# Kernel optimization log

Measured on AMD Instinct MI355X. Metric: run time of the kernel, lower is better.

## Reference

```python
import jax, jax.numpy as jnp
import numpy as np

B, T, E, H, V, A = 128, 31, 512, 512, 10000, 2048


def _lstm_step(h, c, x, W_ih, W_hh, b_ih, b_hh):
    # PyTorch LSTM gate order: i, f, g, o
    gates = x @ W_ih.T + h @ W_hh.T + b_ih + b_hh  # [B, 4H]
    i, f, g, o = jnp.split(gates, 4, axis=-1)
    i = jax.nn.sigmoid(i)
    f = jax.nn.sigmoid(f)
    g = jnp.tanh(g)
    o = jax.nn.sigmoid(o)
    c2 = f * c + i * g
    h2 = o * jnp.tanh(c2)
    return h2, c2


def setup_inputs() -> dict:
    key = jax.random.key(0)
    ks = jax.random.split(key, 16)
    s = 0.1                      # uniform_(-0.1, 0.1) init in the module
    k = 1.0 / np.sqrt(H)         # PyTorch LSTM default init
    u = lambda kk, shape, a: jax.random.uniform(kk, shape, jnp.float32, -a, a)
    return {
        "features": jax.random.normal(ks[0], (B, E), jnp.float32),
        "cnn_features": jax.random.uniform(ks[1], (B, A), jnp.float32),
        "captions": jax.random.randint(ks[2], (B, T), 0, V),
        "lengths": jnp.full((B,), T + 1, dtype=jnp.int32),
        "embed_table": u(ks[3], (V, E), s),
        "W_ih": u(ks[4], (4 * H, E), k),
        "W_hh": u(ks[5], (4 * H, H), k),
        "b_ih": u(ks[6], (4 * H,), k),
        "b_hh": u(ks[7], (4 * H,), k),
        "W_attn": u(ks[8], (A, H + E), s),
        "b_attn": jnp.zeros((A,), jnp.float32),
        "W_attd": u(ks[9], (E, A + E), s),
        "b_attd": jnp.zeros((E,), jnp.float32),
        "W_out": u(ks[10], (V, H), s),
        "b_out": jnp.zeros((V,), jnp.float32),
    }


def reference(features, cnn_features, captions, lengths, embed_table,
              W_ih, W_hh, b_ih, b_hh, W_attn, b_attn, W_attd, b_attd,
              W_out, b_out):
    # embeddings with image feature prepended: [B, T+1, E]
    emb = embed_table[captions]
    xs = jnp.concatenate([features[:, None, :], emb], axis=1)

    # timestep 0: plain LSTM step from zero state (no attention)
    h0 = jnp.zeros((B, H), xs.dtype)
    c0 = jnp.zeros((B, H), xs.dtype)
    h1, c1 = _lstm_step(h0, c0, xs[:, 0], W_ih, W_hh, b_ih, b_hh)

    def step(carry, x_t):
        h, c = carry
        info = jnp.concatenate([x_t, h], axis=-1)                    # [B, E+H]
        aw = jax.nn.softmax(info @ W_attn.T + b_attn, axis=-1)       # [B, 2048]
        attended = cnn_features * aw                                  # [B, 2048]
        x2 = jnp.concatenate([x_t, attended], axis=-1) @ W_attd.T + b_attd  # [B, E]
        h2, c2 = _lstm_step(h, c, x2, W_ih, W_hh, b_ih, b_hh)
        return (h2, c2), h2

    xs_rest = jnp.swapaxes(xs[:, 1:], 0, 1)          # [T, B, E]
    _, hs = jax.lax.scan(step, (h1, c1), xs_rest)    # [T, B, H]

    hidden = jnp.concatenate([h1[None], hs], axis=0)  # [T+1, B, H] packed order
    hidden = hidden.reshape(-1, H)                    # [(T+1)*B, H]
    logits = hidden @ W_out.T + b_out                 # [(T+1)*B, V]
    return logits
```

## Files before the change

### kernel.cpp

```cpp
#include <hip/hip_runtime.h>

#define B_ 128
#define T_ 31
#define E_ 512
#define H_ 512
#define V_ 10000
#define A_ 2048
#define TP1 32
#define G4 2048
#define NHC 4096
#define MPRE 3968

typedef unsigned short u16;
typedef __attribute__((ext_vector_type(8))) short bf16x8;
typedef __attribute__((ext_vector_type(4))) float f32x4;

__device__ __forceinline__ u16 f2b(float f) {
  union { float f; unsigned u; } x; x.f = f;
  unsigned r = x.u + 0x7fffu + ((x.u >> 16) & 1u);
  return (u16)(r >> 16);
}
__device__ __forceinline__ float sigmoidf_(float x) { return 1.f / (1.f + __expf(-x)); }


__global__ __launch_bounds__(256) void prep_xs(
    u16* __restrict__ xs, const float* __restrict__ features,
    const int* __restrict__ captions, const float* __restrict__ embed) {
  int idx = blockIdx.x * 256 + threadIdx.x;
  int e = idx & 511;
  int b = (idx >> 9) & 127;
  int t = idx >> 16;
  float v;
  if (t == 0) v = features[b * 512 + e];
  else        v = embed[(size_t)captions[b * 31 + (t - 1)] * 512 + e];
  xs[idx] = f2b(v);
}

__global__ __launch_bounds__(256) void cast_k(
    u16* __restrict__ dst, const float* __restrict__ src, int n) {
  int i = blockIdx.x * 256 + threadIdx.x;
  if (i < n) dst[i] = f2b(src[i]);
}

__global__ __launch_bounds__(256) void prep_attn_w(
    u16* __restrict__ WattnE, u16* __restrict__ WhComb, const float* __restrict__ W_attn) {
  int i = blockIdx.x * 256 + threadIdx.x;
  int r = i >> 9, k = i & 511;
  WattnE[i] = f2b(W_attn[r * 1024 + k]);
  WhComb[i] = f2b(W_attn[r * 1024 + 512 + k]);
}

__global__ __launch_bounds__(256) void prep_attdE(
    u16* __restrict__ dst, const float* __restrict__ W_attd) {
  int i = blockIdx.x * 256 + threadIdx.x;
  int r = i >> 9, k = i & 511;
  dst[i] = f2b(W_attd[r * 2560 + k]);
}

__global__ __launch_bounds__(256) void prep_attdAT(
    u16* __restrict__ dst, const float* __restrict__ W_attd) {
  int i = blockIdx.x * 256 + threadIdx.x;
  int a = i >> 9, e = i & 511;
  dst[i] = f2b(W_attd[(size_t)e * 2560 + 512 + a]);
}

__global__ __launch_bounds__(256) void add_bias2(
    float* __restrict__ dst, const float* __restrict__ a, const float* __restrict__ b) {
  int i = blockIdx.x * 256 + threadIdx.x;
  if (i < G4) dst[i] = a[i] + b[i];
}

template<bool OUT_BF16, bool ATOMIC, bool NGUARD>
__global__ __launch_bounds__(256) void gemm_nt(
    const u16* __restrict__ Ag, const u16* __restrict__ Bg,
    void* __restrict__ Cout, const float* __restrict__ bias,
    int N, int lda, int ldb, int ldc, int kChunk) {
  __shared__ __align__(16) u16 As[64 * 40];
  __shared__ __align__(16) u16 Bs[64 * 40];
  const int n0 = blockIdx.x * 64;
  const int m0 = blockIdx.y * 64;
  const int k0 = blockIdx.z * kChunk;
  const int tid  = threadIdx.x;
  const int wave = tid >> 6, lane = tid & 63;
  const int quad = lane >> 4, lq = lane & 15;
  const int srow = tid >> 2, sgrp = tid & 3;

  f32x4 acc[4] = {{0,0,0,0},{0,0,0,0},{0,0,0,0},{0,0,0,0}};
  const u16* aptr = Ag + (size_t)(m0 + srow) * lda + k0 + sgrp * 8;
  const u16* bptr = Bg + (size_t)(n0 + srow) * ldb + k0 + sgrp * 8;
  const bool bvalid = !NGUARD || (n0 + srow) < N;

  for (int kk = 0; kk < kChunk; kk += 32) {
    uint4 av = *(const uint4*)(aptr + kk);
    uint4 bv = make_uint4(0u, 0u, 0u, 0u);
    if (bvalid) bv = *(const uint4*)(bptr + kk);
    __syncthreads();
    *(uint4*)&As[srow * 40 + sgrp * 8] = av;
    *(uint4*)&Bs[srow * 40 + sgrp * 8] = bv;
    __syncthreads();
    bf16x8 af = *(const bf16x8*)&As[(wave * 16 + lq) * 40 + quad * 8];
#pragma unroll
    for (int j = 0; j < 4; ++j) {
      bf16x8 bfr = *(const bf16x8*)&Bs[(j * 16 + lq) * 40 + quad * 8];
      acc[j] = __builtin_amdgcn_mfma_f32_16x16x32_bf16(af, bfr, acc[j], 0, 0, 0);
    }
  }
  const int row = m0 + wave * 16 + quad * 4;
#pragma unroll
  for (int j = 0; j < 4; ++j) {
    int col = n0 + j * 16 + lq;
    if (NGUARD && col >= N) continue;
    float bval = bias ? bias[col] : 0.f;
#pragma unroll
    for (int r = 0; r < 4; ++r) {
      float v = acc[j][r] + bval;
      size_t ci = (size_t)(row + r) * ldc + col;
      if (OUT_BF16)      ((u16*)Cout)[ci] = f2b(v);
      else if (ATOMIC)   atomicAdd((float*)Cout + ci, v);
      else               ((float*)Cout)[ci] = v;
    }
  }
}


__global__ __launch_bounds__(256) void attn_softmax(
    const float* __restrict__ preA_t, const float* __restrict__ hW,
    const float* __restrict__ cnn, u16* __restrict__ att, float* __restrict__ g2) {
  int b = blockIdx.x, tid = threadIdx.x;
  float e[8]; float sum = 0.f;
#pragma unroll
  for (int i = 0; i < 8; ++i) {
    int n = tid + i * 256;
    float s = preA_t[b * 2048 + n] + hW[b * 4096 + n];
    e[i] = __expf(s);
    sum += e[i];
  }
#pragma unroll
  for (int o = 32; o > 0; o >>= 1) sum += __shfl_down(sum, o);
  __shared__ float wsum[4];
  if ((tid & 63) == 0) wsum[tid >> 6] = sum;
  __syncthreads();
  float inv = 1.f / (wsum[0] + wsum[1] + wsum[2] + wsum[3]);
#pragma unroll
  for (int i = 0; i < 8; ++i) {
    int n = tid + i * 256;
    att[b * 2048 + n] = f2b(cnn[b * 2048 + n] * e[i] * inv);
    g2[b * 2048 + n] = 0.f;
  }
}

__global__ __launch_bounds__(256) void lstm_pw(
    const float* __restrict__ gA, int ldA,
    const float* __restrict__ gB, const float* __restrict__ gC,
    float* __restrict__ c_st, u16* __restrict__ h_out, int first) {
  int idx = blockIdx.x * 256 + threadIdx.x;
  int b = idx >> 9, j = idx & 511;
  size_t ra = (size_t)b * ldA;
  float gi = gA[ra + j], gf = gA[ra + 512 + j], gg = gA[ra + 1024 + j], go = gA[ra + 1536 + j];
  if (gB) {
    size_t rb = (size_t)b * 4096 + 2048;
    gi += gB[rb + j]; gf += gB[rb + 512 + j]; gg += gB[rb + 1024 + j]; go += gB[rb + 1536 + j];
  }
  if (gC) {
    size_t rc = (size_t)b * 2048;
    gi += gC[rc + j]; gf += gC[rc + 512 + j]; gg += gC[rc + 1024 + j]; go += gC[rc + 1536 + j];
  }
  float iv = sigmoidf_(gi), fv = sigmoidf_(gf), gv = tanhf(gg), ov = sigmoidf_(go);
  float cp = first ? 0.f : c_st[idx];
  float cn = fv * cp + iv * gv;
  c_st[idx] = cn;
  h_out[idx] = f2b(ov * tanhf(cn));
}


extern "C" void kernel_launch(void* const* d_in, const int* in_sizes, int n_in,
                              void* d_out, int out_size, void* d_ws, size_t ws_size,
                              hipStream_t stream) {
  (void)in_sizes; (void)n_in; (void)out_size; (void)ws_size;
  const float* features = (const float*)d_in[0];
  const float* cnn      = (const float*)d_in[1];
  const int*   captions = (const int*)d_in[2];
  const float* embed    = (const float*)d_in[4];
  const float* W_ih     = (const float*)d_in[5];
  const float* W_hh     = (const float*)d_in[6];
  const float* b_ih     = (const float*)d_in[7];
  const float* b_hh     = (const float*)d_in[8];
  const float* W_attn   = (const float*)d_in[9];
  const float* b_attn   = (const float*)d_in[10];
  const float* W_attd   = (const float*)d_in[11];
  const float* b_attd   = (const float*)d_in[12];
  const float* W_out    = (const float*)d_in[13];
  const float* b_out    = (const float*)d_in[14];

  char* ws = (char*)d_ws;
  size_t off = 0;
  auto alloc = [&](size_t bytes) { void* p = ws + off; off += (bytes + 255) & ~255UL; return p; };
  u16*   xs_tb   = (u16*)  alloc((size_t)TP1 * B_ * E_ * 2);
  u16*   h_all   = (u16*)  alloc((size_t)TP1 * B_ * H_ * 2);
  u16*   Wh_comb = (u16*)  alloc((size_t)NHC * H_ * 2);
  u16*   W_ih_b  = (u16*)  alloc((size_t)G4 * E_ * 2);
  u16*   W_attnE = (u16*)  alloc((size_t)A_ * E_ * 2);
  u16*   W_attdE = (u16*)  alloc((size_t)E_ * E_ * 2);
  u16*   W_attdAT= (u16*)  alloc((size_t)A_ * E_ * 2);
  u16*   W_out_b = (u16*)  alloc((size_t)V_ * H_ * 2);
  u16*   Wc      = (u16*)  alloc((size_t)G4 * A_ * 2);
  u16*   pre_x2  = (u16*)  alloc((size_t)MPRE * E_ * 2);
  float* c_st    = (float*)alloc((size_t)B_ * H_ * 4);
  float* hW      = (float*)alloc((size_t)B_ * NHC * 4);
  float* g2      = (float*)alloc((size_t)B_ * G4 * 4);
  u16*   att     = (u16*)  alloc((size_t)B_ * A_ * 2);
  float* bias_c  = (float*)alloc((size_t)G4 * 4);

  float* preA = (float*)d_out;
  float* preG = preA + (size_t)MPRE * A_;
  float* logits = (float*)d_out;

  prep_xs<<<(TP1 * B_ * E_) / 256, 256, 0, stream>>>(xs_tb, features, captions, embed);
  cast_k<<<(G4 * E_) / 256, 256, 0, stream>>>(W_ih_b, W_ih, G4 * E_);
  cast_k<<<(V_ * H_) / 256, 256, 0, stream>>>(W_out_b, W_out, V_ * H_);
  cast_k<<<(G4 * H_) / 256, 256, 0, stream>>>(Wh_comb + (size_t)A_ * H_, W_hh, G4 * H_);
  prep_attn_w<<<(A_ * E_) / 256, 256, 0, stream>>>(W_attnE, Wh_comb, W_attn);
  prep_attdE<<<(E_ * E_) / 256, 256, 0, stream>>>(W_attdE, W_attd);
  prep_attdAT<<<(A_ * E_) / 256, 256, 0, stream>>>(W_attdAT, W_attd);
  add_bias2<<<G4 / 256, 256, 0, stream>>>(bias_c, b_ih, b_hh);

  gemm_nt<true, false, false><<<dim3(A_ / 64, G4 / 64, 1), 256, 0, stream>>>(
      W_ih_b, W_attdAT, Wc, nullptr, A_, 512, 512, A_, 512);
  gemm_nt<false, false, false><<<dim3(A_ / 64, MPRE / 64, 1), 256, 0, stream>>>(
      xs_tb + (size_t)B_ * E_, W_attnE, preA, b_attn, A_, 512, 512, A_, 512);
  gemm_nt<true, false, false><<<dim3(E_ / 64, MPRE / 64, 1), 256, 0, stream>>>(
      xs_tb + (size_t)B_ * E_, W_attdE, pre_x2, b_attd, E_, 512, 512, E_, 512);
  gemm_nt<false, false, false><<<dim3(G4 / 64, MPRE / 64, 1), 256, 0, stream>>>(
      pre_x2, W_ih_b, preG, bias_c, G4, 512, 512, G4, 512);
  gemm_nt<false, false, false><<<dim3(G4 / 64, B_ / 64, 1), 256, 0, stream>>>(
      xs_tb, W_ih_b, g2, bias_c, G4, 512, 512, G4, 512);
  lstm_pw<<<(B_ * H_) / 256, 256, 0, stream>>>(g2, G4, nullptr, nullptr, c_st, h_all, 1);

  for (int t = 1; t <= T_; ++t) {
    gemm_nt<false, false, false><<<dim3(NHC / 64, B_ / 64, 1), 256, 0, stream>>>(
        h_all + (size_t)(t - 1) * B_ * H_, Wh_comb, hW, nullptr, NHC, 512, 512, NHC, 512);
    attn_softmax<<<B_, 256, 0, stream>>>(
        preA + (size_t)(t - 1) * B_ * A_, hW, cnn, att, g2);
    gemm_nt<false, true, false><<<dim3(G4 / 64, B_ / 64, 4), 256, 0, stream>>>(
        att, Wc, g2, nullptr, G4, A_, A_, G4, 512);
    lstm_pw<<<(B_ * H_) / 256, 256, 0, stream>>>(
        preG + (size_t)(t - 1) * B_ * G4, G4, hW, g2, c_st,
        h_all + (size_t)t * B_ * H_, 0);
  }

  gemm_nt<false, false, true><<<dim3((V_ + 63) / 64, (TP1 * B_) / 64, 1), 256, 0, stream>>>(
      h_all, W_out_b, logits, b_out, V_, 512, 512, V_, 512);
}
```

Measured before the change: 1.247 ms.

## Fuse recurrent timestep loop into one persistent kernel with grid barriers

Replaces the 31-step host loop of four launches per step (h GEMM, softmax, attention GEMM with atomics, pointwise LSTM) with a single persistent 256-block kernel. Inside it the steps are separated by software grid barriers on an atomic counter. Gate weights and biases are permuted so each block owns 4 gates of a hidden unit, which lets the attention GEMM reduce through LDS and keep the cell state in registers. This removes about 124 launches and the atomics. The cost is spin-wait barriers, which rely on all 256 blocks being co-resident; this is not guaranteed.

Result: slower. 3.937 ms (+215.7%).

```diff
diff --git a/kernel.cpp b/kernel.cpp
--- a/kernel.cpp
+++ b/kernel.cpp
@@ -42,6 +42,14 @@
   if (i < n) dst[i] = f2b(src[i]);
 }
 
+__global__ __launch_bounds__(256) void prep_w_perm(
+    u16* __restrict__ dst, const float* __restrict__ W) {
+  int i = blockIdx.x * 256 + threadIdx.x;
+  int gp = i >> 9, k = i & 511;
+  int j = gp >> 2, gate = gp & 3;
+  dst[i] = f2b(W[((size_t)gate * 512 + j) * 512 + k]);
+}
+
 __global__ __launch_bounds__(256) void prep_attn_w(
     u16* __restrict__ WattnE, u16* __restrict__ WhComb, const float* __restrict__ W_attn) {
   int i = blockIdx.x * 256 + threadIdx.x;
@@ -64,10 +72,14 @@
   dst[i] = f2b(W_attd[(size_t)e * 2560 + 512 + a]);
 }
 
-__global__ __launch_bounds__(256) void add_bias2(
+__global__ __launch_bounds__(256) void prep_bias_p(
     float* __restrict__ dst, const float* __restrict__ a, const float* __restrict__ b) {
   int i = blockIdx.x * 256 + threadIdx.x;
-  if (i < G4) dst[i] = a[i] + b[i];
+  if (i < G4) {
+    int j = i >> 2, gate = i & 3;
+    int g = gate * 512 + j;
+    dst[i] = a[g] + b[g];
+  }
 }
 
 template<bool OUT_BF16, bool ATOMIC, bool NGUARD>
@@ -122,54 +134,130 @@
   }
 }
 
-
-__global__ __launch_bounds__(256) void attn_softmax(
-    const float* __restrict__ preA_t, const float* __restrict__ hW,
-    const float* __restrict__ cnn, u16* __restrict__ att, float* __restrict__ g2) {
-  int b = blockIdx.x, tid = threadIdx.x;
-  float e[8]; float sum = 0.f;
-#pragma unroll
-  for (int i = 0; i < 8; ++i) {
-    int n = tid + i * 256;
-    float s = preA_t[b * 2048 + n] + hW[b * 4096 + n];
-    e[i] = __expf(s);
-    sum += e[i];
-  }
-#pragma unroll
-  for (int o = 32; o > 0; o >>= 1) sum += __shfl_down(sum, o);
-  __shared__ float wsum[4];
-  if ((tid & 63) == 0) wsum[tid >> 6] = sum;
-  __syncthreads();
-  float inv = 1.f / (wsum[0] + wsum[1] + wsum[2] + wsum[3]);
-#pragma unroll
-  for (int i = 0; i < 8; ++i) {
-    int n = tid + i * 256;
-    att[b * 2048 + n] = f2b(cnn[b * 2048 + n] * e[i] * inv);
-    g2[b * 2048 + n] = 0.f;
-  }
-}
-
-__global__ __launch_bounds__(256) void lstm_pw(
-    const float* __restrict__ gA, int ldA,
-    const float* __restrict__ gB, const float* __restrict__ gC,
-    float* __restrict__ c_st, u16* __restrict__ h_out, int first) {
+__global__ __launch_bounds__(256) void lstm0_pw(
+    const float* __restrict__ g0, float* __restrict__ c_st, u16* __restrict__ h0) {
   int idx = blockIdx.x * 256 + threadIdx.x;
   int b = idx >> 9, j = idx & 511;
-  size_t ra = (size_t)b * ldA;
-  float gi = gA[ra + j], gf = gA[ra + 512 + j], gg = gA[ra + 1024 + j], go = gA[ra + 1536 + j];
-  if (gB) {
-    size_t rb = (size_t)b * 4096 + 2048;
-    gi += gB[rb + j]; gf += gB[rb + 512 + j]; gg += gB[rb + 1024 + j]; go += gB[rb + 1536 + j];
-  }
-  if (gC) {
-    size_t rc = (size_t)b * 2048;
-    gi += gC[rc + j]; gf += gC[rc + 512 + j]; gg += gC[rc + 1024 + j]; go += gC[rc + 1536 + j];
-  }
-  float iv = sigmoidf_(gi), fv = sigmoidf_(gf), gv = tanhf(gg), ov = sigmoidf_(go);
-  float cp = first ? 0.f : c_st[idx];
-  float cn = fv * cp + iv * gv;
-  c_st[idx] = cn;
-  h_out[idx] = f2b(ov * tanhf(cn));
+  float4 g = *(const float4*)&g0[(size_t)b * 2048 + j * 4];
+  float iv = sigmoidf_(g.x), gv = tanhf(g.z), ov = sigmoidf_(g.w);
+  float c = iv * gv;
+  c_st[idx] = c;
+  h0[idx] = f2b(ov * tanhf(c));
+}
+
+
+__device__ __forceinline__ void grid_barrier(unsigned* ctr, unsigned target) {
+  __syncthreads();
+  if (threadIdx.x == 0) {
+    __threadfence();
+    __hip_atomic_fetch_add(ctr, 1u, __ATOMIC_RELAXED, __HIP_MEMORY_SCOPE_AGENT);
+    while (__hip_atomic_load(ctr, __ATOMIC_RELAXED, __HIP_MEMORY_SCOPE_AGENT) < target)
+      __builtin_amdgcn_s_sleep(1);
+  }
+  __syncthreads();
+  __threadfence();
+}
+
+__global__ __launch_bounds__(256) void recurrence(
+    const u16* __restrict__ Whc, const u16* __restrict__ Wc,
+    const float* __restrict__ preA, const float* __restrict__ preG,
+    const float* __restrict__ cnn, const float* __restrict__ c_init,
+    u16* __restrict__ h_all, float* __restrict__ hW, u16* __restrict__ att,
+    unsigned* __restrict__ ctr) {
+  __shared__ float red[4 * 64 * 17];
+  __shared__ float wsum[4];
+  const int w = blockIdx.x;
+  const int tid = threadIdx.x;
+  const int wv = tid >> 6, lane = tid & 63;
+  const int quad = lane >> 4, lq = lane & 15;
+  const int mhalf = w >> 7, cg = w & 127;
+  const int bl = tid >> 2, jj = tid & 3;
+  const int b_own = mhalf * 64 + bl;
+  const int j_own = cg * 4 + jj;
+  float c_reg = c_init[b_own * 512 + j_own];
+  unsigned bar = 0;
+
+  for (int t = 1; t <= T_; ++t) {
+    const u16* hp = h_all + (size_t)(t - 1) * (B_ * H_);
+    {
+      const int n0 = w * 16;
+      const int m0 = wv * 32;
+      const u16* a0 = hp + (size_t)(m0 + lq) * 512 + quad * 8;
+      const u16* a1 = a0 + 16 * 512;
+      const u16* bp = Whc + (size_t)(n0 + lq) * 512 + quad * 8;
+      f32x4 acc0 = {0,0,0,0}, acc1 = {0,0,0,0};
+      for (int kk = 0; kk < 16; ++kk) {
+        bf16x8 bf  = *(const bf16x8*)(bp + kk * 32);
+        bf16x8 af0 = *(const bf16x8*)(a0 + kk * 32);
+        bf16x8 af1 = *(const bf16x8*)(a1 + kk * 32);
+        acc0 = __builtin_amdgcn_mfma_f32_16x16x32_bf16(af0, bf, acc0, 0, 0, 0);
+        acc1 = __builtin_amdgcn_mfma_f32_16x16x32_bf16(af1, bf, acc1, 0, 0, 0);
+      }
+      float* o0 = hW + (size_t)(m0 + quad * 4) * 4096 + n0 + lq;
+#pragma unroll
+      for (int r = 0; r < 4; ++r) o0[(size_t)r * 4096] = acc0[r];
+      float* o1 = hW + (size_t)(m0 + 16 + quad * 4) * 4096 + n0 + lq;
+#pragma unroll
+      for (int r = 0; r < 4; ++r) o1[(size_t)r * 4096] = acc1[r];
+    }
+    grid_barrier(ctr, (++bar) * 256);
+    if (w < 128) {
+      const float* pA  = preA + ((size_t)(t - 1) * 128 + w) * 2048;
+      const float* hWr = hW + (size_t)w * 4096;
+      float e8[8]; float s = 0.f;
+#pragma unroll
+      for (int i = 0; i < 8; ++i) {
+        int n = tid + i * 256;
+        e8[i] = __expf(pA[n] + hWr[n]);
+        s += e8[i];
+      }
+#pragma unroll
+      for (int o = 32; o > 0; o >>= 1) s += __shfl_down(s, o);
+      if (lane == 0) wsum[wv] = s;
+      __syncthreads();
+      float inv = 1.f / (wsum[0] + wsum[1] + wsum[2] + wsum[3]);
+#pragma unroll
+      for (int i = 0; i < 8; ++i) {
+        int n = tid + i * 256;
+        att[(size_t)w * 2048 + n] = f2b(cnn[(size_t)w * 2048 + n] * e8[i] * inv);
+      }
+    }
+    grid_barrier(ctr, (++bar) * 256);
+    {
+      const u16* ab = att + (size_t)(mhalf * 64 + lq) * 2048 + wv * 512 + quad * 8;
+      const u16* bp = Wc + (size_t)(cg * 16 + lq) * 2048 + wv * 512 + quad * 8;
+      f32x4 acc[4] = {{0,0,0,0},{0,0,0,0},{0,0,0,0},{0,0,0,0}};
+      for (int kk = 0; kk < 16; ++kk) {
+        bf16x8 bf = *(const bf16x8*)(bp + kk * 32);
+#pragma unroll
+        for (int mt = 0; mt < 4; ++mt) {
+          bf16x8 af = *(const bf16x8*)(ab + (size_t)mt * 16 * 2048 + kk * 32);
+          acc[mt] = __builtin_amdgcn_mfma_f32_16x16x32_bf16(af, bf, acc[mt], 0, 0, 0);
+        }
+      }
+#pragma unroll
+      for (int mt = 0; mt < 4; ++mt)
+#pragma unroll
+        for (int r = 0; r < 4; ++r)
+          red[(wv * 64 + mt * 16 + quad * 4 + r) * 17 + lq] = acc[mt][r];
+      __syncthreads();
+      float s0 = 0.f, s1 = 0.f, s2 = 0.f, s3 = 0.f;
+#pragma unroll
+      for (int kw = 0; kw < 4; ++kw) {
+        const float* rr = &red[(kw * 64 + bl) * 17 + jj * 4];
+        s0 += rr[0]; s1 += rr[1]; s2 += rr[2]; s3 += rr[3];
+      }
+      const float4 pg = *(const float4*)&preG[((size_t)(t - 1) * 128 + b_own) * 2048 + cg * 16 + jj * 4];
+      const float4 hg = *(const float4*)&hW[(size_t)b_own * 4096 + 2048 + cg * 16 + jj * 4];
+      float iv = sigmoidf_(s0 + pg.x + hg.x);
+      float fv = sigmoidf_(s1 + pg.y + hg.y);
+      float gv = tanhf(s2 + pg.z + hg.z);
+      float ov = sigmoidf_(s3 + pg.w + hg.w);
+      c_reg = fv * c_reg + iv * gv;
+      h_all[(size_t)t * (B_ * H_) + b_own * 512 + j_own] = f2b(ov * tanhf(c_reg));
+    }
+    grid_barrier(ctr, (++bar) * 256);
+  }
 }
 
 
@@ -197,8 +285,8 @@
   auto alloc = [&](size_t bytes) { void* p = ws + off; off += (bytes + 255) & ~255UL; return p; };
   u16*   xs_tb   = (u16*)  alloc((size_t)TP1 * B_ * E_ * 2);
   u16*   h_all   = (u16*)  alloc((size_t)TP1 * B_ * H_ * 2);
-  u16*   Wh_comb = (u16*)  alloc((size_t)NHC * H_ * 2);
-  u16*   W_ih_b  = (u16*)  alloc((size_t)G4 * E_ * 2);
+  u16*   Whc     = (u16*)  alloc((size_t)NHC * H_ * 2);
+  u16*   W_ih_p  = (u16*)  alloc((size_t)G4 * E_ * 2);
   u16*   W_attnE = (u16*)  alloc((size_t)A_ * E_ * 2);
   u16*   W_attdE = (u16*)  alloc((size_t)E_ * E_ * 2);
   u16*   W_attdAT= (u16*)  alloc((size_t)A_ * E_ * 2);
@@ -207,46 +295,38 @@
   u16*   pre_x2  = (u16*)  alloc((size_t)MPRE * E_ * 2);
   float* c_st    = (float*)alloc((size_t)B_ * H_ * 4);
   float* hW      = (float*)alloc((size_t)B_ * NHC * 4);
-  float* g2      = (float*)alloc((size_t)B_ * G4 * 4);
   u16*   att     = (u16*)  alloc((size_t)B_ * A_ * 2);
-  float* bias_c  = (float*)alloc((size_t)G4 * 4);
+  float* bias_p  = (float*)alloc((size_t)G4 * 4);
+  unsigned* ctr  = (unsigned*)alloc(256);
 
   float* preA = (float*)d_out;
   float* preG = preA + (size_t)MPRE * A_;
   float* logits = (float*)d_out;
 
   prep_xs<<<(TP1 * B_ * E_) / 256, 256, 0, stream>>>(xs_tb, features, captions, embed);
-  cast_k<<<(G4 * E_) / 256, 256, 0, stream>>>(W_ih_b, W_ih, G4 * E_);
+  prep_w_perm<<<(G4 * E_) / 256, 256, 0, stream>>>(W_ih_p, W_ih);
+  prep_w_perm<<<(G4 * H_) / 256, 256, 0, stream>>>(Whc + (size_t)A_ * H_, W_hh);
   cast_k<<<(V_ * H_) / 256, 256, 0, stream>>>(W_out_b, W_out, V_ * H_);
-  cast_k<<<(G4 * H_) / 256, 256, 0, stream>>>(Wh_comb + (size_t)A_ * H_, W_hh, G4 * H_);
-  prep_attn_w<<<(A_ * E_) / 256, 256, 0, stream>>>(W_attnE, Wh_comb, W_attn);
+  prep_attn_w<<<(A_ * E_) / 256, 256, 0, stream>>>(W_attnE, Whc, W_attn);
   prep_attdE<<<(E_ * E_) / 256, 256, 0, stream>>>(W_attdE, W_attd);
   prep_attdAT<<<(A_ * E_) / 256, 256, 0, stream>>>(W_attdAT, W_attd);
-  add_bias2<<<G4 / 256, 256, 0, stream>>>(bias_c, b_ih, b_hh);
+  prep_bias_p<<<G4 / 256, 256, 0, stream>>>(bias_p, b_ih, b_hh);
 
   gemm_nt<true, false, false><<<dim3(A_ / 64, G4 / 64, 1), 256, 0, stream>>>(
-      W_ih_b, W_attdAT, Wc, nullptr, A_, 512, 512, A_, 512);
+      W_ih_p, W_attdAT, Wc, nullptr, A_, 512, 512, A_, 512);
   gemm_nt<false, false, false><<<dim3(A_ / 64, MPRE / 64, 1), 256, 0, stream>>>(
       xs_tb + (size_t)B_ * E_, W_attnE, preA, b_attn, A_, 512, 512, A_, 512);
   gemm_nt<true, false, false><<<dim3(E_ / 64, MPRE / 64, 1), 256, 0, stream>>>(
       xs_tb + (size_t)B_ * E_, W_attdE, pre_x2, b_attd, E_, 512, 512, E_, 512);
   gemm_nt<false, false, false><<<dim3(G4 / 64, MPRE / 64, 1), 256, 0, stream>>>(
-      pre_x2, W_ih_b, preG, bias_c, G4, 512, 512, G4, 512);
+      pre_x2, W_ih_p, preG, bias_p, G4, 512, 512, G4, 512);
   gemm_nt<false, false, false><<<dim3(G4 / 64, B_ / 64, 1), 256, 0, stream>>>(
-      xs_tb, W_ih_b, g2, bias_c, G4, 512, 512, G4, 512);
-  lstm_pw<<<(B_ * H_) / 256, 256, 0, stream>>>(g2, G4, nullptr, nullptr, c_st, h_all, 1);
-
-  for (int t = 1; t <= T_; ++t) {
-    gemm_nt<false, false, false><<<dim3(NHC / 64, B_ / 64, 1), 256, 0, stream>>>(
-        h_all + (size_t)(t - 1) * B_ * H_, Wh_comb, hW, nullptr, NHC, 512, 512, NHC, 512);
-    attn_softmax<<<B_, 256, 0, stream>>>(
-        preA + (size_t)(t - 1) * B_ * A_, hW, cnn, att, g2);
-    gemm_nt<false, true, false><<<dim3(G4 / 64, B_ / 64, 4), 256, 0, stream>>>(
-        att, Wc, g2, nullptr, G4, A_, A_, G4, 512);
-    lstm_pw<<<(B_ * H_) / 256, 256, 0, stream>>>(
-        preG + (size_t)(t - 1) * B_ * G4, G4, hW, g2, c_st,
-        h_all + (size_t)t * B_ * H_, 0);
-  }
+      xs_tb, W_ih_p, hW, bias_p, G4, 512, 512, G4, 512);
+  lstm0_pw<<<(B_ * H_) / 256, 256, 0, stream>>>(hW, c_st, h_all);
+
+  hipMemsetAsync(ctr, 0, sizeof(unsigned), stream);
+  recurrence<<<dim3(256), dim3(256), 0, stream>>>(
+      Whc, Wc, preA, preG, cnn, c_st, h_all, hW, att, ctr);
 
   gemm_nt<false, false, true><<<dim3((V_ + 63) / 64, (TP1 * B_) / 64, 1), 256, 0, stream>>>(
       h_all, W_out_b, logits, b_out, V_, 512, 512, V_, 512);
```
